# Optimization experiments

Measured on AMD Instinct MI355X. Metric: run time of the kernel, lower is better.

## Reference

```python
import jax, jax.numpy as jnp
import numpy as np
import math

D_MODEL = 1024
NUM_HEADS = 16
D_K = D_MODEL // NUM_HEADS
SEQ = 2048
BATCH = 2


def setup_inputs() -> dict:
    key = jax.random.key(0)
    ks = jax.random.split(key, 11)
    s = 1.0 / math.sqrt(D_MODEL)
    return {
        "query": jax.random.normal(ks[0], (SEQ, BATCH, D_MODEL), jnp.float32),
        "key": jax.random.normal(ks[1], (SEQ, BATCH, D_MODEL), jnp.float32),
        "value": jax.random.normal(ks[2], (SEQ, BATCH, D_MODEL), jnp.float32),
        "Wq": jax.random.normal(ks[3], (D_MODEL, D_MODEL), jnp.float32) * s,
        "bq": jnp.zeros((D_MODEL,), jnp.float32),
        "Wk": jax.random.normal(ks[4], (D_MODEL, D_MODEL), jnp.float32) * s,
        "bk": jnp.zeros((D_MODEL,), jnp.float32),
        "Wv": jax.random.normal(ks[5], (D_MODEL, D_MODEL), jnp.float32) * s,
        "bv": jnp.zeros((D_MODEL,), jnp.float32),
        "Wo": jax.random.normal(ks[6], (D_MODEL, D_MODEL), jnp.float32) * s,
        "bo": jnp.zeros((D_MODEL,), jnp.float32),
    }


def _split_heads(x):
    # [S, B, D] -> [S, B, H, d_k]
    S, B, _ = x.shape
    return x.reshape(S, B, NUM_HEADS, D_K)


def reference(query, key, value, Wq, bq, Wk, bk, Wv, bv, Wo, bo):
    # torch Linear: y = x @ W.T + b
    q = _split_heads(query @ Wq.T + bq)   # [S,B,H,dk]
    k = _split_heads(key @ Wk.T + bk)
    v = _split_heads(value @ Wv.T + bv)
    # score[q,k,b,h] = sum_d q[q,b,h,d] k[k,b,h,d]
    score = jnp.einsum('qbhd,kbhd->qkbh', q, k) / math.sqrt(D_K)
    attn = jax.nn.softmax(score, axis=1)  # Softmax(dim=1) == over key axis
    out = jnp.einsum('qkbh,kbhd->qbhd', attn, v)  # [S,B,H,dk]
    S, B = out.shape[0], out.shape[1]
    out = out.reshape(S, B, NUM_HEADS * D_K)
    return out @ Wo.T + bo
```

## Files before the change

### kernel.cpp

```cpp
#include <hip/hip_runtime.h>

typedef unsigned short u16;
typedef short s16x8 __attribute__((ext_vector_type(8)));
typedef short s16x4 __attribute__((ext_vector_type(4)));
typedef float f32x4 __attribute__((ext_vector_type(4)));

#define MFMA_BF16(A,B,C) __builtin_amdgcn_mfma_f32_16x16x32_bf16(A,B,C,0,0,0)

#if defined(__has_builtin)
#if __has_builtin(__builtin_amdgcn_mfma_f32_16x16x16bf16_1k)
#define HAVE_MFMA16 1
#define MFMA16(A,B,C) __builtin_amdgcn_mfma_f32_16x16x16bf16_1k(A,B,C,0,0,0)
#endif
#endif

static constexpr int DMODEL = 1024;
static constexpr int SEQn   = 2048;
static constexpr int BATCH  = 2;
static constexpr int NH     = 16;
static constexpr int DKn    = 64;

__device__ __forceinline__ u16 f2bf(float f) {
    unsigned u = __builtin_bit_cast(unsigned, f);
    u += 0x7FFFu + ((u >> 16) & 1u);
    return (u16)(u >> 16);
}

#if defined(__has_builtin)
#if __has_builtin(__builtin_amdgcn_cvt_pk_bf16_f32)
#define HAVE_PKBF16 1
#endif
#endif
#ifdef HAVE_PKBF16
typedef __bf16 bf16x2 __attribute__((ext_vector_type(2)));
__device__ __forceinline__ unsigned pk2bf(float a, float b) {
    bf16x2 t = __builtin_amdgcn_cvt_pk_bf16_f32(a, b);
    return __builtin_bit_cast(unsigned, t);
}
#else
__device__ __forceinline__ unsigned pk2bf(float a, float b) {
    return (unsigned)f2bf(a) | ((unsigned)f2bf(b) << 16);
}
#endif

__device__ __forceinline__ void gld_lds16(const u16* g, u16* l) {
    __builtin_amdgcn_global_load_lds(
        (const __attribute__((address_space(1))) void*)g,
        (__attribute__((address_space(3))) void*)l,
        16, 0, 0);
}

__global__ void cvt_bf16(const float* __restrict__ q, const float* __restrict__ k,
                         const float* __restrict__ v, const float* __restrict__ wq,
                         const float* __restrict__ wk, const float* __restrict__ wv,
                         const float* __restrict__ wo,
                         u16* __restrict__ qb, u16* __restrict__ kb, u16* __restrict__ vb,
                         u16* __restrict__ wqb, u16* __restrict__ wkb, u16* __restrict__ wvb,
                         u16* __restrict__ wob)
{
    const int z = blockIdx.z;
    const float* S; u16* D; size_t n;
    switch (z) {
        case 0: S = q;  D = qb;  n = 4194304; break;
        case 1: S = k;  D = kb;  n = 4194304; break;
        case 2: S = v;  D = vb;  n = 4194304; break;
        case 3: S = wq; D = wqb; n = 1048576; break;
        case 4: S = wk; D = wkb; n = 1048576; break;
        case 5: S = wv; D = wvb; n = 1048576; break;
        default: S = wo; D = wob; n = 1048576; break;
    }
    const size_t i = ((size_t)blockIdx.x * 256 + threadIdx.x) * 8;
    if (i >= n) return;
    float4 a = *(const float4*)(S + i);
    float4 b = *(const float4*)(S + i + 4);
    uint4 pk;
    pk.x = pk2bf(a.x, a.y); pk.y = pk2bf(a.z, a.w);
    pk.z = pk2bf(b.x, b.y); pk.w = pk2bf(b.z, b.w);
    *(uint4*)(D + i) = pk;
}

template<bool FINAL>
__global__ __launch_bounds__(256, 2)
void gemm_bt(const u16* __restrict__ A0, const u16* __restrict__ A1, const u16* __restrict__ A2,
             const u16* __restrict__ W0, const u16* __restrict__ W1, const u16* __restrict__ W2,
             const float* __restrict__ B0, const float* __restrict__ B1, const float* __restrict__ B2,
             void* __restrict__ O0, void* __restrict__ O1, void* __restrict__ O2)
{
    const u16* A; const u16* W; const float* bias; void* Outv;
    const int z = blockIdx.z;
    if (z == 0)      { A = A0; W = W0; bias = B0; Outv = O0; }
    else if (z == 1) { A = A1; W = W1; bias = B1; Outv = O1; }
    else             { A = A2; W = W2; bias = B2; Outv = O2; }

    __shared__ alignas(16) u16 As[128*64];
    __shared__ alignas(16) u16 Bs[128*64];

    const int tid  = threadIdx.x;
    const int wave = tid >> 6, lane = tid & 63;
    const int quad = lane >> 4, col = lane & 15;
    const int wm = wave & 1, wn = wave >> 1;
    const int m0 = blockIdx.y * 128, n0 = blockIdx.x * 128;

    f32x4 acc[4][4];
#pragma unroll
    for (int i = 0; i < 4; ++i)
#pragma unroll
        for (int j = 0; j < 4; ++j) acc[i][j] = f32x4{0.f,0.f,0.f,0.f};

    for (int kt = 0; kt < DMODEL/64; ++kt) {
        if (kt) __syncthreads();
        const int k0 = kt*64;
#pragma unroll
        for (int i = 0; i < 4; ++i) {
            const int chunk = (i*4 + wave)*64 + lane;
            const int row = chunk >> 3;
            const int kk = ((chunk & 7) ^ (row & 7)) * 8;
            gld_lds16(A + (size_t)(m0 + row)*DMODEL + (k0 + kk), &As[(i*4 + wave)*512]);
            gld_lds16(W + (size_t)(n0 + row)*DMODEL + (k0 + kk), &Bs[(i*4 + wave)*512]);
        }
        __syncthreads();
#pragma unroll
        for (int ks = 0; ks < 2; ++ks) {
            s16x8 af[4], bfr[4];
#pragma unroll
            for (int t = 0; t < 4; ++t) {
                const int ra = wm*64 + t*16 + col;
                af[t]  = *(const s16x8*)&As[ra*64 + (((ks*4 + quad) ^ (ra & 7))*8)];
                const int rb = wn*64 + t*16 + col;
                bfr[t] = *(const s16x8*)&Bs[rb*64 + (((ks*4 + quad) ^ (rb & 7))*8)];
            }
#pragma unroll
            for (int i = 0; i < 4; ++i)
#pragma unroll
                for (int j = 0; j < 4; ++j)
                    acc[i][j] = MFMA_BF16(af[i], bfr[j], acc[i][j]);
        }
    }

    float bv[4];
#pragma unroll
    for (int j = 0; j < 4; ++j) bv[j] = bias[n0 + wn*64 + j*16 + col];

#pragma unroll
    for (int i = 0; i < 4; ++i)
#pragma unroll
        for (int j = 0; j < 4; ++j) {
            const int n = n0 + wn*64 + j*16 + col;
#pragma unroll
            for (int r = 0; r < 4; ++r) {
                const int m = m0 + wm*64 + i*16 + quad*4 + r;
                const float v = acc[i][j][r] + bv[j];
                if (FINAL) {
                    ((float*)Outv)[(size_t)m*DMODEL + n] = v;
                } else {
                    const int s = m >> 1, bb = m & 1, h = n >> 6, dd = n & 63;
                    if (z == 2)
                        ((u16*)Outv)[(((size_t)bb*NH + h)*DKn + dd)*SEQn + s] = f2bf(v);
                    else
                        ((u16*)Outv)[(((size_t)bb*NH + h)*SEQn + s)*DKn + dd] = f2bf(v);
                }
            }
        }
}

__global__ __launch_bounds__(256, 4)
void attn_fwd(const u16* __restrict__ Q, const u16* __restrict__ K,
              const u16* __restrict__ Vt, u16* __restrict__ O)
{
    __shared__ alignas(16) u16 Ks[128*64];
    __shared__ alignas(16) u16 Vs[64*128];

    const int qt = blockIdx.x, bh = blockIdx.y;
    const int b = bh >> 4, h = bh & 15;
    const int tid = threadIdx.x;
    const int wave = tid >> 6, lane = tid & 63;
    const int quad = lane >> 4, col = lane & 15;

    const u16* Qh = Q  + (size_t)bh*SEQn*DKn;
    const u16* Kh = K  + (size_t)bh*SEQn*DKn;
    const u16* Vh = Vt + (size_t)bh*DKn*SEQn;

    const int q0 = qt*64 + wave*16;
    s16x8 qf[2];
#pragma unroll
    for (int ks = 0; ks < 2; ++ks)
        qf[ks] = *(const s16x8*)(Qh + (size_t)(q0 + col)*DKn + ks*32 + quad*8);

    f32x4 o[4];
    float mrow = -1e30f, lrow = 0.f;
#pragma unroll
    for (int dt = 0; dt < 4; ++dt) o[dt] = f32x4{0.f,0.f,0.f,0.f};

    constexpr float CSC = 0.125f * 1.44269504f;

    for (int kt = 0; kt < SEQn/128; ++kt) {
        __syncthreads();
#pragma unroll
        for (int i = 0; i < 4; ++i) {
            {
                const int chunk = (i*4 + wave)*64 + lane;
                const int row = chunk >> 3;
                const int kk = ((chunk & 7) ^ (row & 7))*8;
                gld_lds16(Kh + (size_t)(kt*128 + row)*DKn + kk, &Ks[(i*4 + wave)*512]);
            }
            {
                const int chunk = (i*4 + wave)*64 + lane;
                const int d = chunk >> 4;
                const int kk = ((chunk & 15) ^ (d & 15))*8;
                gld_lds16(Vh + (size_t)d*SEQn + kt*128 + kk, &Vs[(i*4 + wave)*512]);
            }
        }
        __syncthreads();

        f32x4 sfr[8];
#pragma unroll
        for (int nt = 0; nt < 8; ++nt) sfr[nt] = f32x4{0.f,0.f,0.f,0.f};
#pragma unroll
        for (int ks = 0; ks < 2; ++ks) {
            s16x8 kf[8];
#pragma unroll
            for (int nt = 0; nt < 8; ++nt) {
                const int key = nt*16 + col;
                kf[nt] = *(const s16x8*)&Ks[key*64 + (((ks*4 + quad) ^ (key & 7))*8)];
            }
#pragma unroll
            for (int nt = 0; nt < 8; ++nt)
                sfr[nt] = MFMA_BF16(kf[nt], qf[ks], sfr[nt]);
        }

        float mx = -1e30f;
#pragma unroll
        for (int nt = 0; nt < 8; ++nt)
#pragma unroll
            for (int r = 0; r < 4; ++r) mx = fmaxf(mx, sfr[nt][r]);
        mx = fmaxf(mx, __shfl_xor(mx, 16));
        mx = fmaxf(mx, __shfl_xor(mx, 32));
        const float mn = fmaxf(mrow, mx);
        const float alpha = __builtin_amdgcn_exp2f((mrow - mn)*CSC);
        const float negmc = -mn*CSC;
        mrow = mn;

        float rsum = 0.f;
        s16x4 pk[8];
#pragma unroll
        for (int nt = 0; nt < 8; ++nt) {
            float p[4];
#pragma unroll
            for (int r = 0; r < 4; ++r) {
                p[r] = __builtin_amdgcn_exp2f(__builtin_fmaf(sfr[nt][r], CSC, negmc));
                rsum += p[r];
            }
            unsigned w[2] = { pk2bf(p[0], p[1]), pk2bf(p[2], p[3]) };
            __builtin_memcpy(&pk[nt], w, 8);
        }
        rsum += __shfl_xor(rsum, 16);
        rsum += __shfl_xor(rsum, 32);
        lrow = lrow*alpha + rsum;
#pragma unroll
        for (int dt = 0; dt < 4; ++dt)
#pragma unroll
            for (int r = 0; r < 4; ++r) o[dt][r] *= alpha;

#ifdef HAVE_MFMA16
#pragma unroll
        for (int c = 0; c < 8; ++c) {
#pragma unroll
            for (int dt = 0; dt < 4; ++dt) {
                const int d = dt*16 + col;
                const s16x4 vfr = *(const s16x4*)&Vs[d*128 + (((c*2 + (quad>>1)) ^ (d & 15))*8) + (quad & 1)*4];
                o[dt] = MFMA16(vfr, pk[c], o[dt]);
            }
        }
#else
        const int a0 = (32*(quad & 1) + col)*4;
#pragma unroll
        for (int ksp = 0; ksp < 4; ++ksp) {
            int pA[2], pB[2];
            __builtin_memcpy(pA, &pk[ksp*2], 8);
            __builtin_memcpy(pB, &pk[ksp*2 + 1], 8);
            int w[4];
#pragma unroll
            for (int hh = 0; hh < 2; ++hh) {
                const int ad = a0 + hh*64;
                const int xA0 = __builtin_amdgcn_ds_bpermute(ad, pA[0]);
                const int xA1 = __builtin_amdgcn_ds_bpermute(ad, pA[1]);
                const int xB0 = __builtin_amdgcn_ds_bpermute(ad, pB[0]);
                const int xB1 = __builtin_amdgcn_ds_bpermute(ad, pB[1]);
                w[hh*2]     = (quad >= 2) ? xB0 : xA0;
                w[hh*2 + 1] = (quad >= 2) ? xB1 : xA1;
            }
            s16x8 pfr; __builtin_memcpy(&pfr, w, 16);
#pragma unroll
            for (int dt = 0; dt < 4; ++dt) {
                const int d = dt*16 + col;
                const s16x8 vfr = *(const s16x8*)&Vs[d*128 + (((ksp*4 + quad) ^ (d & 15))*8)];
                o[dt] = MFMA_BF16(vfr, pfr, o[dt]);
            }
        }
#endif
    }

    const float inv = 1.f / lrow;
    const int srow = q0 + col;
#pragma unroll
    for (int dt = 0; dt < 4; ++dt) {
        uint2 pko;
        pko.x = pk2bf(o[dt][0]*inv, o[dt][1]*inv);
        pko.y = pk2bf(o[dt][2]*inv, o[dt][3]*inv);
        *(uint2*)(O + ((size_t)srow*BATCH + b)*DMODEL + h*DKn + dt*16 + quad*4) = pko;
    }
}

extern "C" void kernel_launch(void* const* d_in, const int* in_sizes, int n_in,
                              void* d_out, int out_size, void* d_ws, size_t ws_size,
                              hipStream_t stream)
{
    const float* q  = (const float*)d_in[0];
    const float* k  = (const float*)d_in[1];
    const float* v  = (const float*)d_in[2];
    const float* Wq = (const float*)d_in[3];
    const float* bq = (const float*)d_in[4];
    const float* Wk = (const float*)d_in[5];
    const float* bk = (const float*)d_in[6];
    const float* Wv = (const float*)d_in[7];
    const float* bv = (const float*)d_in[8];
    const float* Wo = (const float*)d_in[9];
    const float* bo = (const float*)d_in[10];
    float* out = (float*)d_out;

    const size_t N = (size_t)SEQn * BATCH * DMODEL;
    const size_t NW = (size_t)DMODEL * DMODEL;
    u16* qb  = (u16*)d_ws;
    u16* kb  = qb + N;
    u16* vb  = kb + N;
    u16* wqb = vb + N;
    u16* wkb = wqb + NW;
    u16* wvb = wkb + NW;
    u16* wob = wvb + NW;
    u16* Qw  = wob + NW;
    u16* Kw  = Qw + N;
    u16* Vtw = Kw + N;
    u16* AO  = qb;

    cvt_bf16<<<dim3(2048, 1, 7), 256, 0, stream>>>(q, k, v, Wq, Wk, Wv, Wo,
                                                   qb, kb, vb, wqb, wkb, wvb, wob);
    gemm_bt<false><<<dim3(8, 32, 3), 256, 0, stream>>>(qb, kb, vb, wqb, wkb, wvb,
                                                       bq, bk, bv, Qw, Kw, Vtw);
    attn_fwd<<<dim3(32, 32), 256, 0, stream>>>(Qw, Kw, Vtw, AO);
    gemm_bt<true><<<dim3(8, 32, 1), 256, 0, stream>>>(AO, AO, AO, wob, wob, wob,
                                                      bo, bo, bo, out, out, out);
}
```

Measured before the change: 250.0 us.

## Stage QKV projection epilogue through LDS for coalesced vector stores

The non-final GEMM epilogue now writes bf16 results into shared memory and then emits 16-byte vector stores. Q and K stay in the natural [S,B,D] row layout, and the attention kernel reads them with a row stride of BATCH*DMODEL instead of a per-head contiguous layout. V is still transposed, now through LDS, so its global writes are vectorized along the sequence axis. This replaces scattered 2-byte global stores with coalesced wide ones, at the cost of extra syncs and LDS traffic in the epilogue, plus strided Q/K loads in attention.

```diff
diff --git a/kernel.cpp b/kernel.cpp
--- a/kernel.cpp
+++ b/kernel.cpp
@@ -19,6 +19,7 @@
 static constexpr int BATCH  = 2;
 static constexpr int NH     = 16;
 static constexpr int DKn    = 64;
+static constexpr int ROWST  = BATCH*DMODEL;
 
 __device__ __forceinline__ u16 f2bf(float f) {
     unsigned u = __builtin_bit_cast(unsigned, f);
@@ -92,8 +93,9 @@
     else if (z == 1) { A = A1; W = W1; bias = B1; Outv = O1; }
     else             { A = A2; W = W2; bias = B2; Outv = O2; }
 
-    __shared__ alignas(16) u16 As[128*64];
-    __shared__ alignas(16) u16 Bs[128*64];
+    __shared__ alignas(16) u16 SH[128*128];
+    u16* As = SH;
+    u16* Bs = SH + 128*64;
 
     const int tid  = threadIdx.x;
     const int wave = tid >> 6, lane = tid & 63;
@@ -141,26 +143,59 @@
 #pragma unroll
     for (int j = 0; j < 4; ++j) bv[j] = bias[n0 + wn*64 + j*16 + col];
 
-#pragma unroll
-    for (int i = 0; i < 4; ++i)
-#pragma unroll
-        for (int j = 0; j < 4; ++j) {
-            const int n = n0 + wn*64 + j*16 + col;
-#pragma unroll
-            for (int r = 0; r < 4; ++r) {
-                const int m = m0 + wm*64 + i*16 + quad*4 + r;
-                const float v = acc[i][j][r] + bv[j];
-                if (FINAL) {
-                    ((float*)Outv)[(size_t)m*DMODEL + n] = v;
-                } else {
-                    const int s = m >> 1, bb = m & 1, h = n >> 6, dd = n & 63;
-                    if (z == 2)
-                        ((u16*)Outv)[(((size_t)bb*NH + h)*DKn + dd)*SEQn + s] = f2bf(v);
-                    else
-                        ((u16*)Outv)[(((size_t)bb*NH + h)*SEQn + s)*DKn + dd] = f2bf(v);
+    if (FINAL) {
+#pragma unroll
+        for (int i = 0; i < 4; ++i)
+#pragma unroll
+            for (int j = 0; j < 4; ++j) {
+                const int n = n0 + wn*64 + j*16 + col;
+#pragma unroll
+                for (int r = 0; r < 4; ++r) {
+                    const int m = m0 + wm*64 + i*16 + quad*4 + r;
+                    ((float*)Outv)[(size_t)m*DMODEL + n] = acc[i][j][r] + bv[j];
                 }
             }
-        }
+    } else {
+        __syncthreads();
+#pragma unroll
+        for (int i = 0; i < 4; ++i)
+#pragma unroll
+            for (int j = 0; j < 4; ++j) {
+                const int nl = wn*64 + j*16 + col;
+#pragma unroll
+                for (int r = 0; r < 4; ++r) {
+                    const int ml = wm*64 + i*16 + quad*4 + r;
+                    SH[ml*128 + nl] = f2bf(acc[i][j][r] + bv[j]);
+                }
+            }
+        __syncthreads();
+        u16* Out = (u16*)Outv;
+        if (z < 2) {
+#pragma unroll
+            for (int t = 0; t < 8; ++t) {
+                const int c = t*256 + tid;
+                const int ml = c >> 4, n8 = (c & 15)*8;
+                uint4 x = *(const uint4*)&SH[ml*128 + n8];
+                *(uint4*)(Out + (size_t)(m0 + ml)*DMODEL + n0 + n8) = x;
+            }
+        } else {
+            const int s0 = m0 >> 1;
+#pragma unroll
+            for (int t = 0; t < 8; ++t) {
+                const int c = t*256 + tid;
+                const int nl = c & 127;
+                const int g = c >> 7;
+                const int bb = g >> 3, sc = g & 7;
+                u16 e[8];
+#pragma unroll
+                for (int j = 0; j < 8; ++j)
+                    e[j] = SH[((sc*8 + j)*2 + bb)*128 + nl];
+                uint4 x; __builtin_memcpy(&x, e, 16);
+                const int ng = n0 + nl, hh = ng >> 6, dd = ng & 63;
+                *(uint4*)(Out + (((size_t)bb*NH + hh)*DKn + dd)*SEQn + s0 + sc*8) = x;
+            }
+        }
+    }
 }
 
 __global__ __launch_bounds__(256, 4)
@@ -176,15 +211,15 @@
     const int wave = tid >> 6, lane = tid & 63;
     const int quad = lane >> 4, col = lane & 15;
 
-    const u16* Qh = Q  + (size_t)bh*SEQn*DKn;
-    const u16* Kh = K  + (size_t)bh*SEQn*DKn;
+    const u16* Qh = Q + b*DMODEL + h*DKn;
+    const u16* Kh = K + b*DMODEL + h*DKn;
     const u16* Vh = Vt + (size_t)bh*DKn*SEQn;
 
     const int q0 = qt*64 + wave*16;
     s16x8 qf[2];
 #pragma unroll
     for (int ks = 0; ks < 2; ++ks)
-        qf[ks] = *(const s16x8*)(Qh + (size_t)(q0 + col)*DKn + ks*32 + quad*8);
+        qf[ks] = *(const s16x8*)(Qh + (size_t)(q0 + col)*ROWST + ks*32 + quad*8);
 
     f32x4 o[4];
     float mrow = -1e30f, lrow = 0.f;
@@ -201,7 +236,7 @@
                 const int chunk = (i*4 + wave)*64 + lane;
                 const int row = chunk >> 3;
                 const int kk = ((chunk & 7) ^ (row & 7))*8;
-                gld_lds16(Kh + (size_t)(kt*128 + row)*DKn + kk, &Ks[(i*4 + wave)*512]);
+                gld_lds16(Kh + (size_t)(kt*128 + row)*ROWST + kk, &Ks[(i*4 + wave)*512]);
             }
             {
                 const int chunk = (i*4 + wave)*64 + lane;
```

New measurement: 242.2 us. 1.03x faster.
